# Performance work log

Measured on AMD Instinct MI355X. Metric: run time of the kernel, lower is better.

## Reference

```python
import jax, jax.numpy as jnp
import numpy as np

L, T, B, H = 2, 512, 64, 1024


def setup_inputs() -> dict:
    key = jax.random.key(0)
    ks = jax.random.split(key, 6)
    std = 1.0 / np.sqrt(H)
    uni = lambda k, shp: jax.random.uniform(k, shp, jnp.float32, -std, std)
    return {
        "x": jax.random.normal(ks[0], (T, B, H), jnp.float32),
        "h0": jnp.zeros((L, B, H), jnp.float32),
        "c0": jnp.zeros((L, B, H), jnp.float32),
        "i2h_w": uni(ks[1], (L, 4 * H, H)),
        "i2h_b": uni(ks[2], (L, 4 * H)),
        "h2h_w": uni(ks[3], (L, 4 * H, H)),
        "h2h_b": uni(ks[4], (L, 4 * H)),
    }


def _layer(x_seq, h, c, Wi, bi, Wh, bh):
    # Precompute input projection for all timesteps: [T, B, 4H]
    xp = jnp.einsum('tbi,gi->tbg', x_seq, Wi) + bi

    def step(carry, xp_t):
        h, c = carry
        preact = xp_t + h @ Wh.T + bh          # [B, 4H]
        ig, fg, gg, og = jnp.split(preact, 4, axis=-1)
        ig = jax.nn.sigmoid(ig)
        fg = jax.nn.sigmoid(fg)
        gg = jnp.tanh(gg)
        og = jax.nn.sigmoid(og)
        c = c * fg + ig * gg
        h = og * jnp.tanh(c)
        return (h, c), (h, c)

    _, (hs, cs) = jax.lax.scan(step, (h, c), xp)
    return hs, cs  # each [T, B, H]


def reference(x, h0, c0, i2h_w, i2h_b, h2h_w, h2h_b):
    output_hs, output_cs = [], []
    hs = x
    for l in range(L):
        hs, cs = _layer(hs, h0[l], c0[l], i2h_w[l], i2h_b[l], h2h_w[l], h2h_b[l])
        # dropout=0 so dropout layer is identity
        output_hs.append(hs[-1])
        # NOTE: original code has a bug: appends hs[-1] for cs too; replicated.
        output_cs.append(hs[-1])
    output_hs = jnp.stack(output_hs, axis=0)  # [L, B, H]
    output_cs = jnp.stack(output_cs, axis=0)
    return (hs, (output_hs, output_cs))
```

## Files before the change

### kernel.cpp

```cpp
#include <hip/hip_runtime.h>
#include <hip/hip_bf16.h>
#include <math.h>


#define Hh 1024
#define Bb 64
#define Tt 512
#define BH (Bb*Hh)
#define G4 (4*Hh)

typedef __bf16 v8bf __attribute__((ext_vector_type(8)));
typedef float  v4f  __attribute__((ext_vector_type(4)));
typedef unsigned long long u64;
typedef __hip_bfloat16 bf16;

__device__ __forceinline__ bf16 f2bf(float v){ return __float2bfloat16(v); }

__device__ __forceinline__ v8bf cvt8(const float* p) {
    v4f a = *(const v4f*)p;
    v4f b = *(const v4f*)(p + 4);
    v8bf r;
    #pragma unroll
    for (int i = 0; i < 4; ++i) {
        r[i]   = __builtin_bit_cast(__bf16, f2bf(a[i]));
        r[i+4] = __builtin_bit_cast(__bf16, f2bf(b[i]));
    }
    return r;
}

__device__ __forceinline__ float fast_sigmoid(float x) {
    x = fminf(fmaxf(x, -30.f), 30.f);
    return 1.f / (1.f + __expf(-x));
}
__device__ __forceinline__ float fast_tanh(float x) {
    x = fminf(fmaxf(x, -15.f), 15.f);
    float e = __expf(2.f * x);
    return (e - 1.f) / (e + 1.f);
}

#define ISS4(buf, base) do {                                                   \
    asm volatile("global_load_dwordx4 %0, %1, off sc0 sc1"                     \
                 : "=v"(buf[0]) : "v"(ap + (base+0)*32));                      \
    asm volatile("global_load_dwordx4 %0, %1, off sc0 sc1"                     \
                 : "=v"(buf[1]) : "v"(ap + (base+1)*32));                      \
    asm volatile("global_load_dwordx4 %0, %1, off sc0 sc1"                     \
                 : "=v"(buf[2]) : "v"(ap + (base+2)*32));                      \
    asm volatile("global_load_dwordx4 %0, %1, off sc0 sc1"                     \
                 : "=v"(buf[3]) : "v"(ap + (base+3)*32));                      \
} while (0)

#define MFMA4(buf, base) do {                                                  \
    _Pragma("unroll")                                                          \
    for (int k = 0; k < 4; ++k) {                                              \
        acc0 = __builtin_amdgcn_mfma_f32_16x16x32_bf16(buf[k], Breg[(base)+k][0], acc0, 0,0,0); \
        acc1 = __builtin_amdgcn_mfma_f32_16x16x32_bf16(buf[k], Breg[(base)+k][1], acc1, 0,0,0); \
    }                                                                          \
} while (0)

__global__ void init_ws(const float* __restrict__ h0,
                        bf16* __restrict__ hout, unsigned int* __restrict__ bar) {
    int i = blockIdx.x * blockDim.x + threadIdx.x;
    if (i < 256) bar[i] = 0u;
    hout[(0*2 + 1)*BH + i] = f2bf(h0[i]);
    hout[(1*2 + 0)*BH + i] = f2bf(h0[BH + i]);
}

__global__ __launch_bounds__(1024, 4)
void lstm_persist(const float* __restrict__ x,
                  const float* __restrict__ wi, const float* __restrict__ bi,
                  const float* __restrict__ wh, const float* __restrict__ bh,
                  const float* __restrict__ c0,
                  bf16* __restrict__ hout,
                  float* __restrict__ out, unsigned int* __restrict__ bar)
{
    const int layer  = blockIdx.x >> 7;
    const int jslice = blockIdx.x & 127;
    const int jbase  = jslice * 8;

    const int tid  = threadIdx.x;
    const int lane = tid & 63;
    const int w    = tid >> 6;
    const int ks   = w >> 3;
    const int kh   = (w >> 2) & 1;
    const int rt   = w & 3;
    const int s    = w >> 2;
    const int quad = lane >> 4;
    const int l15  = lane & 15;

    const float* W = (ks ? wh : wi) + (size_t)layer * G4 * Hh;
    v8bf Breg[16][2];
    #pragma unroll
    for (int ct = 0; ct < 2; ++ct) {
        const int n    = ct*16 + l15;
        const int grow = (n >> 3)*Hh + jbase + (n & 7);
        const float* wp = W + (size_t)grow * Hh + kh*512 + quad*8;
        #pragma unroll
        for (int kk = 0; kk < 16; ++kk)
            Breg[kk][ct] = cvt8(wp + kk*32);
    }

    const int arow = rt*16 + l15;
    const size_t aoff = (size_t)arow * Hh + kh*512 + quad*8;

    const int eb  = tid >> 2;
    const int ejp = tid & 3;
    float bsum[4][2];
    float c_reg[2] = {0.f, 0.f};
    if (tid < 256) {
        #pragma unroll
        for (int gi = 0; gi < 4; ++gi) {
            #pragma unroll
            for (int u = 0; u < 2; ++u) {
                int bo = layer*G4 + gi*Hh + jbase + 2*ejp + u;
                bsum[gi][u] = bi[bo] + bh[bo];
            }
        }
        #pragma unroll
        for (int u = 0; u < 2; ++u)
            c_reg[u] = c0[(size_t)layer*BH + eb*Hh + jbase + 2*ejp + u];
    }

    __shared__ float part[4][64][36];

    for (int p = 0; p <= Tt; ++p) {
        const int t = p - layer;
        const bool act = (t >= 0) & (t < Tt);

        if (act) {
            v4f acc0 = {0.f,0.f,0.f,0.f}, acc1 = {0.f,0.f,0.f,0.f};
            if (ks == 0 && layer == 0) {
                const float* ap = x + (size_t)t*BH + aoff;
                #pragma unroll
                for (int kk = 0; kk < 16; ++kk) {
                    v8bf af = cvt8(ap + kk*32);
                    acc0 = __builtin_amdgcn_mfma_f32_16x16x32_bf16(af, Breg[kk][0], acc0, 0,0,0);
                    acc1 = __builtin_amdgcn_mfma_f32_16x16x32_bf16(af, Breg[kk][1], acc1, 0,0,0);
                }
            } else {
                const int srcbuf = (ks == 0) ? ((p-1) & 1)
                                             : (layer*2 + ((p-1) & 1));
                const bf16* ap = hout + (size_t)srcbuf*BH + aoff;
                v8bf afA[4], afB[4];
                ISS4(afA, 0);
                ISS4(afB, 4);
                asm volatile("s_waitcnt vmcnt(4)");
                __builtin_amdgcn_sched_barrier(0);
                MFMA4(afA, 0);
                __builtin_amdgcn_sched_barrier(0);
                ISS4(afA, 8);
                asm volatile("s_waitcnt vmcnt(4)");
                __builtin_amdgcn_sched_barrier(0);
                MFMA4(afB, 4);
                __builtin_amdgcn_sched_barrier(0);
                ISS4(afB, 12);
                asm volatile("s_waitcnt vmcnt(4)");
                __builtin_amdgcn_sched_barrier(0);
                MFMA4(afA, 8);
                __builtin_amdgcn_sched_barrier(0);
                asm volatile("s_waitcnt vmcnt(0)");
                __builtin_amdgcn_sched_barrier(0);
                MFMA4(afB, 12);
            }
            #pragma unroll
            for (int r = 0; r < 4; ++r) {
                part[s][rt*16 + quad*4 + r][l15]      = acc0[r];
                part[s][rt*16 + quad*4 + r][16 + l15] = acc1[r];
            }
        }
        __syncthreads();

        if (tid < 256 && act) {
            float g[4][2];
            #pragma unroll
            for (int gi = 0; gi < 4; ++gi) {
                int c = gi*8 + 2*ejp;
                g[gi][0] = part[0][eb][c]   + part[1][eb][c]
                         + part[2][eb][c]   + part[3][eb][c]   + bsum[gi][0];
                g[gi][1] = part[0][eb][c+1] + part[1][eb][c+1]
                         + part[2][eb][c+1] + part[3][eb][c+1] + bsum[gi][1];
            }
            float hv[2];
            #pragma unroll
            for (int u = 0; u < 2; ++u) {
                float ig = fast_sigmoid(g[0][u]);
                float fg = fast_sigmoid(g[1][u]);
                float gv = fast_tanh(g[2][u]);
                float og = fast_sigmoid(g[3][u]);
                c_reg[u] = c_reg[u]*fg + ig*gv;
                hv[u] = og * fast_tanh(c_reg[u]);
            }

            const int idx = eb*Hh + jbase + 2*ejp;
            unsigned int hp =
                  (unsigned int)__builtin_bit_cast(unsigned short, f2bf(hv[0]))
                | ((unsigned int)__builtin_bit_cast(unsigned short, f2bf(hv[1])) << 16);
            __hip_atomic_store((unsigned int*)(hout + (size_t)(layer*2 + (p & 1))*BH + idx),
                               hp, __ATOMIC_RELAXED, __HIP_MEMORY_SCOPE_AGENT);
            if (layer == 1) {
                float2 o; o.x = hv[0]; o.y = hv[1];
                *(float2*)(out + (size_t)t*BH + idx) = o;
            }
            if (t == Tt-1) {
                float2 o; o.x = hv[0]; o.y = hv[1];
                *(float2*)(out + (size_t)Tt*BH + (size_t)layer*BH + idx)       = o;
                *(float2*)(out + (size_t)Tt*BH + (size_t)(2 + layer)*BH + idx) = o;
            }
        }

        if (p < Tt) {
            __syncthreads();
            if (w == 0) {
                if (lane == 0)
                    __hip_atomic_fetch_add(bar + (blockIdx.x & 15)*16, 1u,
                                           __ATOMIC_RELAXED, __HIP_MEMORY_SCOPE_AGENT);
                const unsigned int tgt = (unsigned int)(p + 1) * 16u;
                bool done = (lane >= 16);
                while (!__all(done)) {
                    if (!done)
                        done = (__hip_atomic_load(bar + lane*16, __ATOMIC_RELAXED,
                                                  __HIP_MEMORY_SCOPE_AGENT) >= tgt);
                    if (!__all(done))
                        __builtin_amdgcn_s_sleep(2);
                }
            }
            __syncthreads();
        }
    }
}

extern "C" void kernel_launch(void* const* d_in, const int* in_sizes, int n_in,
                              void* d_out, int out_size, void* d_ws, size_t ws_size,
                              hipStream_t stream) {
    const float* x  = (const float*)d_in[0];
    const float* h0 = (const float*)d_in[1];
    const float* c0 = (const float*)d_in[2];
    const float* wi = (const float*)d_in[3];
    const float* bi = (const float*)d_in[4];
    const float* wh = (const float*)d_in[5];
    const float* bh = (const float*)d_in[6];
    float* out = (float*)d_out;

    char* ws = (char*)d_ws;
    unsigned int* bar = (unsigned int*)ws;
    bf16* hout = (bf16*)(ws + 1024);

    init_ws<<<256, 256, 0, stream>>>(h0, hout, bar);
    lstm_persist<<<256, 1024, 0, stream>>>(x, wi, bi, wh, bh, c0,
                                           hout, out, bar);
}
```

Before: 12.50 ms.

## Halve persistent grid by giving each block sixteen hidden units

```diff
diff --git a/kernel.cpp b/kernel.cpp
--- a/kernel.cpp
+++ b/kernel.cpp
@@ -49,11 +49,13 @@
                  : "=v"(buf[3]) : "v"(ap + (base+3)*32));                      \
 } while (0)
 
-#define MFMA4(buf, base) do {                                                  \
+#define MFMA16(buf, base) do {                                                 \
     _Pragma("unroll")                                                          \
     for (int k = 0; k < 4; ++k) {                                              \
-        acc0 = __builtin_amdgcn_mfma_f32_16x16x32_bf16(buf[k], Breg[(base)+k][0], acc0, 0,0,0); \
-        acc1 = __builtin_amdgcn_mfma_f32_16x16x32_bf16(buf[k], Breg[(base)+k][1], acc1, 0,0,0); \
+        _Pragma("unroll")                                                      \
+        for (int ct = 0; ct < 4; ++ct)                                         \
+            acc[ct] = __builtin_amdgcn_mfma_f32_16x16x32_bf16(                 \
+                buf[k], Breg[(base)+k][ct], acc[ct], 0,0,0);                   \
     }                                                                          \
 } while (0)
 
@@ -73,9 +75,9 @@
                   bf16* __restrict__ hout,
                   float* __restrict__ out, unsigned int* __restrict__ bar)
 {
-    const int layer  = blockIdx.x >> 7;
-    const int jslice = blockIdx.x & 127;
-    const int jbase  = jslice * 8;
+    const int layer  = blockIdx.x >> 6;
+    const int jslice = blockIdx.x & 63;
+    const int jbase  = jslice * 16;
 
     const int tid  = threadIdx.x;
     const int lane = tid & 63;
@@ -88,11 +90,10 @@
     const int l15  = lane & 15;
 
     const float* W = (ks ? wh : wi) + (size_t)layer * G4 * Hh;
-    v8bf Breg[16][2];
+    v8bf Breg[16][4];
     #pragma unroll
-    for (int ct = 0; ct < 2; ++ct) {
-        const int n    = ct*16 + l15;
-        const int grow = (n >> 3)*Hh + jbase + (n & 7);
+    for (int ct = 0; ct < 4; ++ct) {
+        const int grow = ct*Hh + jbase + l15;
         const float* wp = W + (size_t)grow * Hh + kh*512 + quad*8;
         #pragma unroll
         for (int kk = 0; kk < 16; ++kk)
@@ -102,11 +103,11 @@
     const int arow = rt*16 + l15;
     const size_t aoff = (size_t)arow * Hh + kh*512 + quad*8;
 
-    const int eb  = tid >> 2;
-    const int ejp = tid & 3;
+    const int eb  = tid >> 3;
+    const int ejp = tid & 7;
     float bsum[4][2];
     float c_reg[2] = {0.f, 0.f};
-    if (tid < 256) {
+    if (tid < 512) {
         #pragma unroll
         for (int gi = 0; gi < 4; ++gi) {
             #pragma unroll
@@ -120,21 +121,26 @@
             c_reg[u] = c0[(size_t)layer*BH + eb*Hh + jbase + 2*ejp + u];
     }
 
-    __shared__ float part[4][64][36];
+    __shared__ float part[4][64][68];
 
     for (int p = 0; p <= Tt; ++p) {
         const int t = p - layer;
         const bool act = (t >= 0) & (t < Tt);
 
         if (act) {
-            v4f acc0 = {0.f,0.f,0.f,0.f}, acc1 = {0.f,0.f,0.f,0.f};
+            v4f acc[4];
+            #pragma unroll
+            for (int ct = 0; ct < 4; ++ct) acc[ct] = (v4f){0.f,0.f,0.f,0.f};
+
             if (ks == 0 && layer == 0) {
                 const float* ap = x + (size_t)t*BH + aoff;
                 #pragma unroll
                 for (int kk = 0; kk < 16; ++kk) {
                     v8bf af = cvt8(ap + kk*32);
-                    acc0 = __builtin_amdgcn_mfma_f32_16x16x32_bf16(af, Breg[kk][0], acc0, 0,0,0);
-                    acc1 = __builtin_amdgcn_mfma_f32_16x16x32_bf16(af, Breg[kk][1], acc1, 0,0,0);
+                    #pragma unroll
+                    for (int ct = 0; ct < 4; ++ct)
+                        acc[ct] = __builtin_amdgcn_mfma_f32_16x16x32_bf16(
+                            af, Breg[kk][ct], acc[ct], 0,0,0);
                 }
             } else {
                 const int srcbuf = (ks == 0) ? ((p-1) & 1)
@@ -145,35 +151,36 @@
                 ISS4(afB, 4);
                 asm volatile("s_waitcnt vmcnt(4)");
                 __builtin_amdgcn_sched_barrier(0);
-                MFMA4(afA, 0);
+                MFMA16(afA, 0);
                 __builtin_amdgcn_sched_barrier(0);
                 ISS4(afA, 8);
                 asm volatile("s_waitcnt vmcnt(4)");
                 __builtin_amdgcn_sched_barrier(0);
-                MFMA4(afB, 4);
+                MFMA16(afB, 4);
                 __builtin_amdgcn_sched_barrier(0);
                 ISS4(afB, 12);
                 asm volatile("s_waitcnt vmcnt(4)");
                 __builtin_amdgcn_sched_barrier(0);
-                MFMA4(afA, 8);
+                MFMA16(afA, 8);
                 __builtin_amdgcn_sched_barrier(0);
                 asm volatile("s_waitcnt vmcnt(0)");
                 __builtin_amdgcn_sched_barrier(0);
-                MFMA4(afB, 12);
+                MFMA16(afB, 12);
             }
             #pragma unroll
             for (int r = 0; r < 4; ++r) {
-                part[s][rt*16 + quad*4 + r][l15]      = acc0[r];
-                part[s][rt*16 + quad*4 + r][16 + l15] = acc1[r];
+                #pragma unroll
+                for (int ct = 0; ct < 4; ++ct)
+                    part[s][rt*16 + quad*4 + r][ct*16 + l15] = acc[ct][r];
             }
         }
         __syncthreads();
 
-        if (tid < 256 && act) {
+        if (tid < 512 && act) {
             float g[4][2];
             #pragma unroll
             for (int gi = 0; gi < 4; ++gi) {
-                int c = gi*8 + 2*ejp;
+                int c = gi*16 + 2*ejp;
                 g[gi][0] = part[0][eb][c]   + part[1][eb][c]
                          + part[2][eb][c]   + part[3][eb][c]   + bsum[gi][0];
                 g[gi][1] = part[0][eb][c+1] + part[1][eb][c+1]
@@ -213,7 +220,7 @@
                 if (lane == 0)
                     __hip_atomic_fetch_add(bar + (blockIdx.x & 15)*16, 1u,
                                            __ATOMIC_RELAXED, __HIP_MEMORY_SCOPE_AGENT);
-                const unsigned int tgt = (unsigned int)(p + 1) * 16u;
+                const unsigned int tgt = (unsigned int)(p + 1) * 8u;
                 bool done = (lane >= 16);
                 while (!__all(done)) {
                     if (!done)
@@ -245,6 +252,6 @@
     bf16* hout = (bf16*)(ws + 1024);
 
     init_ws<<<256, 256, 0, stream>>>(h0, hout, bar);
-    lstm_persist<<<256, 1024, 0, stream>>>(x, wi, bi, wh, bh, c0,
+    lstm_persist<<<128, 1024, 0, stream>>>(x, wi, bi, wh, bh, c0,
                                            hout, out, bar);
 }
```

Result: slower. 20.93 ms (+67.4%).
